# Performance work log

Hardware: AMD Instinct MI355X
Metric: run time of the kernel (lower is better)

## Reference

```python
import jax, jax.numpy as jnp
import numpy as np

NUM_CLASSES = 100000
FEAT_DIM = 512
BATCH = 32768
ALPHA1 = 1.0
ALPHA2 = 50.0  # alpha * 50
A_CONST = 0.2
WARMUP = 15
EPS = 1e-12  # torch F.normalize eps


def setup_inputs() -> dict:
    key = jax.random.key(0)
    k1, k2, k3, k4 = jax.random.split(key, 4)
    x = jax.random.normal(k1, (BATCH, FEAT_DIM), dtype=jnp.float32)
    labels = jax.random.randint(k2, (BATCH,), 0, NUM_CLASSES, dtype=jnp.int64)
    ori_labels = jax.random.randint(k3, (BATCH,), 0, NUM_CLASSES, dtype=jnp.int64)
    centers = jax.random.normal(k4, (NUM_CLASSES, FEAT_DIM), dtype=jnp.float32)
    return {"x": x, "labels": labels, "ori_labels": ori_labels, "epoch": 5, "centers": centers}


def _l2norm(v, axis):
    # matches torch F.normalize(p=2): divide by max(||v||, eps)
    n = jnp.sqrt(jnp.sum(v * v, axis=axis, keepdims=True))
    return v / jnp.maximum(n, EPS)


def reference(x, labels, ori_labels, epoch, centers):
    C = centers.shape[0]
    xn = _l2norm(x, axis=1)                      # [B, D]
    cn = _l2norm(centers, axis=1)                # [C, D]

    all_centers_mean = jnp.sum(cn, axis=0) / C   # [D]
    s_all = xn @ all_centers_mean                # [B]  dot(x, mean of all centers)

    # one-hot multiply-and-sum == direct gather of the label's center
    c_lab = cn[labels]                           # [B, D]
    s_lab = jnp.sum(c_lab * xn, axis=1)          # [B]

    e_all = jnp.exp(s_all)
    # first branch scales the gathered center by (C+1)/C before the dot
    loss_1 = jnp.mean((e_all - jnp.exp(s_lab * ((C + 1.0) / C))) / ALPHA1)
    loss_2 = jnp.mean(-jnp.abs((e_all - jnp.exp(s_lab) + A_CONST) / ALPHA2))

    v = min(epoch / (WARMUP - 1), 1)             # epoch is a Python int
    loss = (1.0 - v) * loss_1 + v * loss_2
    return (loss, centers)
```

## Files before the change

### kernel.cpp

```cpp
#include <hip/hip_runtime.h>
#include <math.h>

#define C_CLASSES 100000
#define FEAT      512
#define BATCH_N   32768
#define EPS_N     1e-12f

__global__ void __launch_bounds__(256) centers_pass(
    const float* __restrict__ centers,
    float* __restrict__ out,
    float* __restrict__ cpart,
    float* __restrict__ rnorms)
{
    const int t   = threadIdx.x;
    const int wid = t >> 6;
    const int ln  = t & 63;
    const int nb  = gridDim.x;

    float acc[8] = {0.f,0.f,0.f,0.f,0.f,0.f,0.f,0.f};

    for (int row = blockIdx.x * 4 + wid; row < C_CLASSES; row += nb * 4) {
        const size_t rbase = (size_t)row * FEAT;
        const float4* rp4 = reinterpret_cast<const float4*>(centers + rbase);

        const float4 v0 = rp4[ln];
        const float4 v1 = rp4[ln + 64];

        const float prev_row = (row > 0) ? centers[rbase - 1] : 0.f;

        float ss = v0.x*v0.x + v0.y*v0.y + v0.z*v0.z + v0.w*v0.w
                 + v1.x*v1.x + v1.y*v1.y + v1.z*v1.z + v1.w*v1.w;
        #pragma unroll
        for (int o = 32; o > 0; o >>= 1) ss += __shfl_xor(ss, o, 64);

        const float rn = 1.f / fmaxf(sqrtf(ss), EPS_N);
        if (ln == 0) rnorms[row] = rn;

        acc[0] += v0.x * rn; acc[1] += v0.y * rn; acc[2] += v0.z * rn; acc[3] += v0.w * rn;
        acc[4] += v1.x * rn; acc[5] += v1.y * rn; acc[6] += v1.z * rn; acc[7] += v1.w * rn;

        const float w0up = __shfl_up(v0.w, 1, 64);
        const float w1up = __shfl_up(v1.w, 1, 64);
        const float w063 = __shfl(v0.w, 63, 64);

        float4* op4 = reinterpret_cast<float4*>(out + rbase);
        const float4 s0 = make_float4((ln == 0) ? prev_row : w0up, v0.x, v0.y, v0.z);
        const float4 s1 = make_float4((ln == 0) ? w063     : w1up, v1.x, v1.y, v1.z);

        if (row == 0 && ln == 0) {
            out[1] = s0.y; out[2] = s0.z; out[3] = s0.w;
        } else {
            op4[ln] = s0;
        }
        op4[ln + 64] = s1;
    }

    __shared__ float accsh[4][FEAT];
    #pragma unroll
    for (int k = 0; k < 8; ++k) accsh[wid][(k & 3) * 4 + (k >> 2) * 256 + 0] = 0.f;
    accsh[wid][4*ln + 0] = acc[0]; accsh[wid][4*ln + 1] = acc[1];
    accsh[wid][4*ln + 2] = acc[2]; accsh[wid][4*ln + 3] = acc[3];
    accsh[wid][256 + 4*ln + 0] = acc[4]; accsh[wid][256 + 4*ln + 1] = acc[5];
    accsh[wid][256 + 4*ln + 2] = acc[6]; accsh[wid][256 + 4*ln + 3] = acc[7];
    __syncthreads();

    #pragma unroll
    for (int j = t; j < FEAT; j += 256)
        cpart[(size_t)blockIdx.x * FEAT + j] =
            accsh[0][j] + accsh[1][j] + accsh[2][j] + accsh[3][j];
}

__global__ void __launch_bounds__(512) reduce_mean_s1(
    const float* __restrict__ cpart, int nblk,
    float* __restrict__ partial2)
{
    const int j = threadIdx.x;
    float s = 0.f;
    for (int b = blockIdx.x; b < nblk; b += gridDim.x)
        s += cpart[(size_t)b * FEAT + j];
    partial2[(size_t)blockIdx.x * FEAT + j] = s;
}

__global__ void __launch_bounds__(512) reduce_mean_s2(
    const float* __restrict__ partial2, int np,
    float* __restrict__ mean)
{
    const int j = threadIdx.x;
    float s = 0.f;
    for (int p = 0; p < np; ++p)
        s += partial2[(size_t)p * FEAT + j];
    mean[j] = s / (float)C_CLASSES;
}

__global__ void __launch_bounds__(256) row_loss(
    const float* __restrict__ x,
    const int*   __restrict__ labels,
    const float* __restrict__ centers,
    const float* __restrict__ mean,
    const float* __restrict__ rnorms,
    float* __restrict__ lpart)
{
    const int wid = threadIdx.x >> 6;
    const int ln  = threadIdx.x & 63;
    const int row = blockIdx.x * 4 + wid;

    const float4* __restrict__ xr = reinterpret_cast<const float4*>(x + (size_t)row * FEAT);
    const float4* __restrict__ mr = reinterpret_cast<const float4*>(mean);
    const int lab = labels[row];
    const float4* __restrict__ cr = reinterpret_cast<const float4*>(centers + (size_t)lab * FEAT);
    const float rnc = rnorms[lab];

    const float4 xv0 = xr[ln], xv1 = xr[ln + 64];
    const float4 mv0 = mr[ln], mv1 = mr[ln + 64];
    const float4 cv0 = cr[ln], cv1 = cr[ln + 64];

    float ssx = xv0.x*xv0.x + xv0.y*xv0.y + xv0.z*xv0.z + xv0.w*xv0.w
              + xv1.x*xv1.x + xv1.y*xv1.y + xv1.z*xv1.z + xv1.w*xv1.w;
    float dxm = xv0.x*mv0.x + xv0.y*mv0.y + xv0.z*mv0.z + xv0.w*mv0.w
              + xv1.x*mv1.x + xv1.y*mv1.y + xv1.z*mv1.z + xv1.w*mv1.w;
    float dxc = xv0.x*cv0.x + xv0.y*cv0.y + xv0.z*cv0.z + xv0.w*cv0.w
              + xv1.x*cv1.x + xv1.y*cv1.y + xv1.z*cv1.z + xv1.w*cv1.w;

    #pragma unroll
    for (int o = 32; o > 0; o >>= 1) {
        ssx += __shfl_xor(ssx, o, 64);
        dxm += __shfl_xor(dxm, o, 64);
        dxc += __shfl_xor(dxc, o, 64);
    }

    __shared__ float t1s[4], t2s[4];
    if (ln == 0) {
        const float rnx = 1.f / fmaxf(sqrtf(ssx), EPS_N);
        const float s_all = dxm * rnx;
        const float s_lab = dxc * rnx * rnc;
        const float e_all = expf(s_all);
        const float kC    = (float)((double)(C_CLASSES + 1) / (double)C_CLASSES);
        const float t1 = (e_all - expf(s_lab * kC));
        const float t2 = -fabsf((e_all - expf(s_lab) + 0.2f) * (1.f / 50.f));
        t1s[wid] = t1;
        t2s[wid] = t2;
    }
    __syncthreads();
    if (threadIdx.x == 0) {
        lpart[(size_t)blockIdx.x * 2]     = t1s[0] + t1s[1] + t1s[2] + t1s[3];
        lpart[(size_t)blockIdx.x * 2 + 1] = t2s[0] + t2s[1] + t2s[2] + t2s[3];
    }
}

__global__ void final_loss(const float* __restrict__ lpart, int n,
                           const int* __restrict__ epoch,
                           const float* __restrict__ centers,
                           float* __restrict__ out)
{
    __shared__ double sh1[256];
    __shared__ double sh2[256];
    double s1 = 0.0, s2 = 0.0;
    for (int i = threadIdx.x; i < n; i += blockDim.x) {
        s1 += (double)lpart[(size_t)i * 2];
        s2 += (double)lpart[(size_t)i * 2 + 1];
    }
    sh1[threadIdx.x] = s1;
    sh2[threadIdx.x] = s2;
    __syncthreads();
    for (int s = 128; s > 0; s >>= 1) {
        if (threadIdx.x < s) {
            sh1[threadIdx.x] += sh1[threadIdx.x + s];
            sh2[threadIdx.x] += sh2[threadIdx.x + s];
        }
        __syncthreads();
    }
    if (threadIdx.x == 0) {
        const float v  = fminf((float)(*epoch) * (1.f / 14.f), 1.f);
        const float l1 = (float)(sh1[0] / (double)BATCH_N);
        const float l2 = (float)(sh2[0] / (double)BATCH_N);
        out[0] = (1.f - v) * l1 + v * l2;
    }
    if (threadIdx.x == 1) {
        const size_t g = (size_t)C_CLASSES * FEAT;
        out[g] = centers[g - 1];
    }
}

extern "C" void kernel_launch(void* const* d_in, const int* in_sizes, int n_in,
                              void* d_out, int out_size, void* d_ws, size_t ws_size,
                              hipStream_t stream)
{
    const float* x       = (const float*)d_in[0];
    const int*   labels  = (const int*)d_in[1];
    const int*   epoch   = (const int*)d_in[3];
    const float* centers = (const float*)d_in[4];
    float* out = (float*)d_out;

    float* ws       = (float*)d_ws;
    float* mean     = ws;
    float* partial2 = ws + 512;
    float* lpart    = ws + 512 + 16384;
    float* rnorms   = ws + 512 + 16384 + 16384;
    float* cpart    = rnorms + 100352;

    const size_t fixed_bytes = (size_t)(512 + 16384 + 16384 + 100352) * sizeof(float);
    int nblkA = 2048;
    if (ws_size < fixed_bytes + (size_t)nblkA * FEAT * sizeof(float)) {
        size_t avail = (ws_size > fixed_bytes) ? (ws_size - fixed_bytes) : 0;
        nblkA = (int)(avail / (FEAT * sizeof(float)));
        if (nblkA < 1) nblkA = 1;
    }

    centers_pass<<<nblkA, 256, 0, stream>>>(centers, out, cpart, rnorms);
    reduce_mean_s1<<<32, 512, 0, stream>>>(cpart, nblkA, partial2);
    reduce_mean_s2<<<1, 512, 0, stream>>>(partial2, 32, mean);
    row_loss<<<BATCH_N / 4, 256, 0, stream>>>(x, labels, centers, mean, rnorms, lpart);
    final_loss<<<1, 256, 0, stream>>>(lpart, BATCH_N / 4, epoch, centers, out);
}
```

Before: 132.0 us.

## Replace multi-stage partial reductions with fixed-point atomic accumulation into slots

Block partial sums for the center mean and the loss terms are now accumulated with 64-bit fixed-point atomics into a small set of striped slots, instead of being written out and reduced by separate kernels. This removes the two-stage mean reduction kernels and shrinks the final loss reduction to a single thread. It also moves the output shift store ahead of the norm computation. A memset launch is added, and the fixed-point scaling trades float precision for deterministic integer sums.

After: 122.3 us. 1.08x faster.

```diff
diff --git a/kernel.cpp b/kernel.cpp
--- a/kernel.cpp
+++ b/kernel.cpp
@@ -5,11 +5,15 @@
 #define FEAT      512
 #define BATCH_N   32768
 #define EPS_N     1e-12f
+#define NBLKA     2048
+#define MSLOTS    32
+#define LSLOTS    64
+#define FIX_SCALE 4294967296.0
 
 __global__ void __launch_bounds__(256) centers_pass(
     const float* __restrict__ centers,
     float* __restrict__ out,
-    float* __restrict__ cpart,
+    unsigned long long* __restrict__ mslots,
     float* __restrict__ rnorms)
 {
     const int t   = threadIdx.x;
@@ -25,8 +29,21 @@
 
         const float4 v0 = rp4[ln];
         const float4 v1 = rp4[ln + 64];
+        const float prev_row = (row > 0) ? centers[rbase - 1] : 0.f;
 
-        const float prev_row = (row > 0) ? centers[rbase - 1] : 0.f;
+        const float w0up = __shfl_up(v0.w, 1, 64);
+        const float w1up = __shfl_up(v1.w, 1, 64);
+        const float w063 = __shfl(v0.w, 63, 64);
+
+        float4* op4 = reinterpret_cast<float4*>(out + rbase);
+        const float4 s0 = make_float4((ln == 0) ? prev_row : w0up, v0.x, v0.y, v0.z);
+        const float4 s1 = make_float4((ln == 0) ? w063     : w1up, v1.x, v1.y, v1.z);
+        if (row == 0 && ln == 0) {
+            out[1] = s0.y; out[2] = s0.z; out[3] = s0.w;
+        } else {
+            op4[ln] = s0;
+        }
+        op4[ln + 64] = s1;
 
         float ss = v0.x*v0.x + v0.y*v0.y + v0.z*v0.z + v0.w*v0.w
                  + v1.x*v1.x + v1.y*v1.y + v1.z*v1.z + v1.w*v1.w;
@@ -38,58 +55,33 @@
 
         acc[0] += v0.x * rn; acc[1] += v0.y * rn; acc[2] += v0.z * rn; acc[3] += v0.w * rn;
         acc[4] += v1.x * rn; acc[5] += v1.y * rn; acc[6] += v1.z * rn; acc[7] += v1.w * rn;
-
-        const float w0up = __shfl_up(v0.w, 1, 64);
-        const float w1up = __shfl_up(v1.w, 1, 64);
-        const float w063 = __shfl(v0.w, 63, 64);
-
-        float4* op4 = reinterpret_cast<float4*>(out + rbase);
-        const float4 s0 = make_float4((ln == 0) ? prev_row : w0up, v0.x, v0.y, v0.z);
-        const float4 s1 = make_float4((ln == 0) ? w063     : w1up, v1.x, v1.y, v1.z);
-
-        if (row == 0 && ln == 0) {
-            out[1] = s0.y; out[2] = s0.z; out[3] = s0.w;
-        } else {
-            op4[ln] = s0;
-        }
-        op4[ln + 64] = s1;
     }
 
     __shared__ float accsh[4][FEAT];
-    #pragma unroll
-    for (int k = 0; k < 8; ++k) accsh[wid][(k & 3) * 4 + (k >> 2) * 256 + 0] = 0.f;
     accsh[wid][4*ln + 0] = acc[0]; accsh[wid][4*ln + 1] = acc[1];
     accsh[wid][4*ln + 2] = acc[2]; accsh[wid][4*ln + 3] = acc[3];
     accsh[wid][256 + 4*ln + 0] = acc[4]; accsh[wid][256 + 4*ln + 1] = acc[5];
     accsh[wid][256 + 4*ln + 2] = acc[6]; accsh[wid][256 + 4*ln + 3] = acc[7];
     __syncthreads();
 
-    #pragma unroll
-    for (int j = t; j < FEAT; j += 256)
-        cpart[(size_t)blockIdx.x * FEAT + j] =
-            accsh[0][j] + accsh[1][j] + accsh[2][j] + accsh[3][j];
+    const int slot = (blockIdx.x & (MSLOTS - 1)) * FEAT;
+    for (int j = t; j < FEAT; j += 256) {
+        const float v = accsh[0][j] + accsh[1][j] + accsh[2][j] + accsh[3][j];
+        const long long q = llrint((double)v * FIX_SCALE);
+        atomicAdd(&mslots[slot + j], (unsigned long long)q);
+    }
 }
 
-__global__ void __launch_bounds__(512) reduce_mean_s1(
-    const float* __restrict__ cpart, int nblk,
-    float* __restrict__ partial2)
-{
-    const int j = threadIdx.x;
-    float s = 0.f;
-    for (int b = blockIdx.x; b < nblk; b += gridDim.x)
-        s += cpart[(size_t)b * FEAT + j];
-    partial2[(size_t)blockIdx.x * FEAT + j] = s;
-}
-
-__global__ void __launch_bounds__(512) reduce_mean_s2(
-    const float* __restrict__ partial2, int np,
+__global__ void __launch_bounds__(512) mean_fin(
+    const unsigned long long* __restrict__ mslots,
     float* __restrict__ mean)
 {
     const int j = threadIdx.x;
-    float s = 0.f;
-    for (int p = 0; p < np; ++p)
-        s += partial2[(size_t)p * FEAT + j];
-    mean[j] = s / (float)C_CLASSES;
+    long long s = 0;
+    #pragma unroll
+    for (int p = 0; p < MSLOTS; ++p)
+        s += (long long)mslots[(size_t)p * FEAT + j];
+    mean[j] = (float)((double)s * (1.0 / FIX_SCALE) / (double)C_CLASSES);
 }
 
 __global__ void __launch_bounds__(256) row_loss(
@@ -98,7 +90,7 @@
     const float* __restrict__ centers,
     const float* __restrict__ mean,
     const float* __restrict__ rnorms,
-    float* __restrict__ lpart)
+    unsigned long long* __restrict__ lslots)
 {
     const int wid = threadIdx.x >> 6;
     const int ln  = threadIdx.x & 63;
@@ -135,44 +127,33 @@
         const float s_lab = dxc * rnx * rnc;
         const float e_all = expf(s_all);
         const float kC    = (float)((double)(C_CLASSES + 1) / (double)C_CLASSES);
-        const float t1 = (e_all - expf(s_lab * kC));
-        const float t2 = -fabsf((e_all - expf(s_lab) + 0.2f) * (1.f / 50.f));
-        t1s[wid] = t1;
-        t2s[wid] = t2;
+        t1s[wid] = (e_all - expf(s_lab * kC));
+        t2s[wid] = -fabsf((e_all - expf(s_lab) + 0.2f) * (1.f / 50.f));
     }
     __syncthreads();
     if (threadIdx.x == 0) {
-        lpart[(size_t)blockIdx.x * 2]     = t1s[0] + t1s[1] + t1s[2] + t1s[3];
-        lpart[(size_t)blockIdx.x * 2 + 1] = t2s[0] + t2s[1] + t2s[2] + t2s[3];
+        const double b1 = (double)t1s[0] + t1s[1] + t1s[2] + t1s[3];
+        const double b2 = (double)t2s[0] + t2s[1] + t2s[2] + t2s[3];
+        const int slot = (blockIdx.x & (LSLOTS - 1)) * 2;
+        atomicAdd(&lslots[slot + 0], (unsigned long long)llrint(b1 * FIX_SCALE));
+        atomicAdd(&lslots[slot + 1], (unsigned long long)llrint(b2 * FIX_SCALE));
     }
 }
 
-__global__ void final_loss(const float* __restrict__ lpart, int n,
-                           const int* __restrict__ epoch,
-                           const float* __restrict__ centers,
-                           float* __restrict__ out)
+__global__ void loss_fin(const unsigned long long* __restrict__ lslots,
+                         const int* __restrict__ epoch,
+                         const float* __restrict__ centers,
+                         float* __restrict__ out)
 {
-    __shared__ double sh1[256];
-    __shared__ double sh2[256];
-    double s1 = 0.0, s2 = 0.0;
-    for (int i = threadIdx.x; i < n; i += blockDim.x) {
-        s1 += (double)lpart[(size_t)i * 2];
-        s2 += (double)lpart[(size_t)i * 2 + 1];
-    }
-    sh1[threadIdx.x] = s1;
-    sh2[threadIdx.x] = s2;
-    __syncthreads();
-    for (int s = 128; s > 0; s >>= 1) {
-        if (threadIdx.x < s) {
-            sh1[threadIdx.x] += sh1[threadIdx.x + s];
-            sh2[threadIdx.x] += sh2[threadIdx.x + s];
+    if (threadIdx.x == 0) {
+        long long q1 = 0, q2 = 0;
+        for (int p = 0; p < LSLOTS; ++p) {
+            q1 += (long long)lslots[(size_t)p * 2 + 0];
+            q2 += (long long)lslots[(size_t)p * 2 + 1];
         }
-        __syncthreads();
-    }
-    if (threadIdx.x == 0) {
         const float v  = fminf((float)(*epoch) * (1.f / 14.f), 1.f);
-        const float l1 = (float)(sh1[0] / (double)BATCH_N);
-        const float l2 = (float)(sh2[0] / (double)BATCH_N);
+        const float l1 = (float)((double)q1 * (1.0 / FIX_SCALE) / (double)BATCH_N);
+        const float l2 = (float)((double)q2 * (1.0 / FIX_SCALE) / (double)BATCH_N);
         out[0] = (1.f - v) * l1 + v * l2;
     }
     if (threadIdx.x == 1) {
@@ -191,24 +172,18 @@
     const float* centers = (const float*)d_in[4];
     float* out = (float*)d_out;
 
-    float* ws       = (float*)d_ws;
-    float* mean     = ws;
-    float* partial2 = ws + 512;
-    float* lpart    = ws + 512 + 16384;
-    float* rnorms   = ws + 512 + 16384 + 16384;
-    float* cpart    = rnorms + 100352;
+    float* ws = (float*)d_ws;
+    float* mean = ws;
+    unsigned long long* mslots = (unsigned long long*)(ws + 512);
+    unsigned long long* lslots = mslots + (size_t)MSLOTS * FEAT;
+    float* rnorms = ws + 512 + 2 * (MSLOTS * FEAT + LSLOTS * 2);
 
-    const size_t fixed_bytes = (size_t)(512 + 16384 + 16384 + 100352) * sizeof(float);
-    int nblkA = 2048;
-    if (ws_size < fixed_bytes + (size_t)nblkA * FEAT * sizeof(float)) {
-        size_t avail = (ws_size > fixed_bytes) ? (ws_size - fixed_bytes) : 0;
-        nblkA = (int)(avail / (FEAT * sizeof(float)));
-        if (nblkA < 1) nblkA = 1;
-    }
+    hipMemsetAsync(mslots, 0,
+                   (size_t)(MSLOTS * FEAT + LSLOTS * 2) * sizeof(unsigned long long),
+                   stream);
 
-    centers_pass<<<nblkA, 256, 0, stream>>>(centers, out, cpart, rnorms);
-    reduce_mean_s1<<<32, 512, 0, stream>>>(cpart, nblkA, partial2);
-    reduce_mean_s2<<<1, 512, 0, stream>>>(partial2, 32, mean);
-    row_loss<<<BATCH_N / 4, 256, 0, stream>>>(x, labels, centers, mean, rnorms, lpart);
-    final_loss<<<1, 256, 0, stream>>>(lpart, BATCH_N / 4, epoch, centers, out);
+    centers_pass<<<NBLKA, 256, 0, stream>>>(centers, out, mslots, rnorms);
+    mean_fin<<<1, 512, 0, stream>>>(mslots, mean);
+    row_loss<<<BATCH_N / 4, 256, 0, stream>>>(x, labels, centers, mean, rnorms, lslots);
+    loss_fin<<<1, 64, 0, stream>>>(lslots, epoch, centers, out);
 }
```
